# Optimization experiments

Hardware: AMD Instinct MI355X
Metric: run time of the kernel (lower is better)

Reference implementation:

```python
import jax, jax.numpy as jnp
import numpy as np

jax.config.update("jax_enable_x64", True)

C = 62          # in/conv channels
T = 2000        # time samples
B = 256         # batch
VEC_DIM = C * (C + 1) // 2  # 1953
HIDDEN = 64
NUM_CLASSES = 3
SPD_EPS = 1e-3
LOGMAP_EPS = 1e-6


def setup_inputs() -> dict:
    key = jax.random.key(0)
    ks = jax.random.split(key, 8)
    x = jax.random.normal(ks[0], (B, C, T), dtype=jnp.float32)
    # Conv1d kernel_size=1 == per-timestep channel mixing: weight [out_c, in_c]
    conv_w = jax.random.normal(ks[1], (C, C), dtype=jnp.float32) / np.sqrt(C)
    conv_b = jax.random.normal(ks[2], (C,), dtype=jnp.float32) * 0.01
    proj_w = jax.random.normal(ks[3], (HIDDEN, VEC_DIM), dtype=jnp.float32) / np.sqrt(VEC_DIM)
    proj_b = jax.random.normal(ks[4], (HIDDEN,), dtype=jnp.float32) * 0.01
    head_w = jax.random.normal(ks[5], (NUM_CLASSES, HIDDEN), dtype=jnp.float32) / np.sqrt(HIDDEN)
    head_b = jax.random.normal(ks[6], (NUM_CLASSES,), dtype=jnp.float32) * 0.01
    return {"x": x, "conv_w": conv_w, "conv_b": conv_b,
            "proj_w": proj_w, "proj_b": proj_b,
            "head_w": head_w, "head_b": head_b}


def _forward(x, conv_w, conv_b, proj_w, proj_b, head_w, head_b):
    # Conv1d with kernel_size=1: [B,C,T] -> [B,C,T]
    xc = jnp.einsum('oc,bct->bot', conv_w, x) + conv_b[None, :, None]
    # covariance in double precision (torch code does .double())
    xc64 = xc.astype(jnp.float64)
    x_cen = xc64 - xc64.mean(axis=2, keepdims=True)
    denom = float(max(1, T - 1))
    cov = jnp.einsum('bct,bdt->bcd', x_cen, x_cen) / denom  # [B,C,C]
    cov = 0.5 * (cov + jnp.swapaxes(cov, 1, 2))
    # SPD regularization + re-symmetrize
    cov = cov + SPD_EPS * jnp.eye(C, dtype=jnp.float64)
    cov = 0.5 * (cov + jnp.swapaxes(cov, 1, 2))
    # log-map: eigh, clamp, log, reconstruct
    vals, vecs = jnp.linalg.eigh(cov)                       # [B,C], [B,C,C]
    log_vals = jnp.log(jnp.maximum(vals, LOGMAP_EPS))
    log_cov = jnp.einsum('bik,bk,bjk->bij', vecs, log_vals, vecs)
    # upper-triangular (incl. diag) vectorization, row-major like torch.triu_indices
    iu, ju = jnp.triu_indices(C)
    vec = log_cov[:, iu, ju].astype(jnp.float32)            # [B, 1953]
    feat = jax.nn.relu(vec @ proj_w.T + proj_b)             # [B, 64]
    logits = feat @ head_w.T + head_b                       # [B, 3]
    return logits


def reference(x, conv_w, conv_b, proj_w, proj_b, head_w, head_b):
    return _forward(x, conv_w, conv_b, proj_w, proj_b, head_w, head_b)
```

## Files before the change

kernel.cpp:

```cpp
#include <hip/hip_runtime.h>
#include <math.h>

#define CC 62
#define TT 2000
#define BB 256
#define VECN 1953
#define HID 64
#define NCLS 3
#define NG 31
#define LDX 68
#define XBUF (64 * LDX)
#define NT1 32
#define SLD 64
#define LDGF 68

typedef const unsigned int __attribute__((address_space(1)))* gbl_u32p;
typedef unsigned int __attribute__((address_space(3)))* lds_u32p;

#define WAITV(n) asm volatile("s_waitcnt vmcnt(" #n ")" ::: "memory")

__device__ __forceinline__ void decodePi(int pi, int& i, int& j)
{
    int ii = 0, rem = pi;
    while (rem >= CC - ii) { rem -= (CC - ii); ++ii; }
    i = ii; j = ii + rem;
}

__device__ __forceinline__ void pairPQ(int r, int k, int& p, int& q)
{
    if (k == 0) { p = 0; q = 1 + (r + 60) % 61; }
    else {
        p = 1 + (r + k - 1) % 61;
        q = 1 + (r + 60 - k) % 61;
    }
    if (p > q) { int t = p; p = q; q = t; }
}

__global__ __launch_bounds__(576) void fused(
    const float* __restrict__ x, const float* __restrict__ cw,
    const float* __restrict__ pw, const float* __restrict__ pbias,
    const float* __restrict__ hw, const float* __restrict__ hb,
    float* __restrict__ out)
{
    const int b = blockIdx.x, tid = threadIdx.x;
    const int wid = tid >> 6, lane = tid & 63;

    __shared__ __align__(16) double sA[4352];
    __shared__ __align__(16) double sC[VECN];
    __shared__ double sU[9 * 64];
    __shared__ double sNorm[64];
    __shared__ double sD[64];
    __shared__ double sMean[64];
    __shared__ unsigned short sPair[61 * NG];
    __shared__ int    sFlag;
    __shared__ float  sF[HID];

    float*  sX   = reinterpret_cast<float*>(sA);
    double* sS   = sA;
    float*  sGf  = reinterpret_cast<float*>(sA);
    float*  sVec = reinterpret_cast<float*>(sC);

    const int slot = tid >> 2, myks = tid & 3;
    const bool actA = (slot < 136);
    int gi = 0, gj = 0;
    if (actA) {
        int g = 0, rem = slot;
        while (rem >= 16 - g) { rem -= (16 - g); ++g; }
        gi = g; gj = g + rem;
    }
    const int a0 = 4 * gi, b0 = 4 * gj;
    const int pA = gi >> 1, pB = gj >> 1;

    double acc[4][4];
    float  accf[4][4];
#pragma unroll
    for (int r = 0; r < 4; ++r)
#pragma unroll
        for (int c = 0; c < 4; ++c) { acc[r][c] = 0.0; accf[r][c] = 0.0f; }

    for (int e = tid; e < 61 * NG; e += 576) {
        int r = e / NG, k = e - r * NG;
        int p, q; pairPQ(r, k, p, q);
        sPair[e] = (unsigned short)(p | (q << 8));
    }
    if (tid < 128) {
        int bu = tid >> 6, t = tid & 63;
        sX[bu * XBUF + 62 * LDX + t] = 1.0f;
        sX[bu * XBUF + 63 * LDX + t] = 0.0f;
    }
    __syncthreads();

    const float* xb = x + (size_t)b * (CC * TT);

    auto issueTile = [&](int buf, int tile) {
        const int t0 = tile * 64;
        for (int c = wid; c < CC; c += 9) {
            const int ps = c >> 3;
            const int tt = 4 * ((lane >> 2) ^ ps) + (lane & 3);
            if (t0 + tt < TT) {
                const float* gp = xb + (size_t)c * TT + t0 + tt;
                __builtin_amdgcn_global_load_lds(
                    (gbl_u32p)gp, (lds_u32p)&sX[buf * XBUF + c * LDX], 4, 0, 0);
            }
        }
    };

    issueTile(0, 0);
    for (int tile = 0; tile < NT1; ++tile) {
        const int cur = tile & 1;
        __builtin_amdgcn_s_barrier();
        if (tile + 1 < NT1) {
            issueTile(cur ^ 1, tile + 1);
            if (wid < 8) WAITV(7); else WAITV(6);
        } else {
            WAITV(0);
        }
        __builtin_amdgcn_sched_barrier(0);
        __builtin_amdgcn_s_barrier();
        if (actA) {
            const float* xt = &sX[cur * XBUF];
            const int nq = min(16, (TT - tile * 64) >> 2);
            for (int m = myks; m < nq; m += 4) {
                const int ca = 4 * (m ^ pA), cb = 4 * (m ^ pB);
                float4 af[4], bf[4];
#pragma unroll
                for (int r = 0; r < 4; ++r)
                    af[r] = *reinterpret_cast<const float4*>(&xt[(a0 + r) * LDX + ca]);
#pragma unroll
                for (int r = 0; r < 4; ++r)
                    bf[r] = *reinterpret_cast<const float4*>(&xt[(b0 + r) * LDX + cb]);
#pragma unroll
                for (int k = 0; k < 4; ++k) {
#pragma unroll
                    for (int r = 0; r < 4; ++r)
#pragma unroll
                        for (int s = 0; s < 4; ++s)
                            accf[r][s] += (&af[r].x)[k] * (&bf[s].x)[k];
                }
            }
#pragma unroll
            for (int r = 0; r < 4; ++r)
#pragma unroll
                for (int c = 0; c < 4; ++c) {
                    acc[r][c] += (double)accf[r][c];
                    accf[r][c] = 0.0f;
                }
        }
    }

#pragma unroll
    for (int r = 0; r < 4; ++r)
#pragma unroll
        for (int c = 0; c < 4; ++c) {
            double v = acc[r][c];
            v += __shfl_xor(v, 1, 4);
            v += __shfl_xor(v, 2, 4);
            acc[r][c] = v;
        }
    __syncthreads();
    if (actA && myks == 0) {
#pragma unroll
        for (int r = 0; r < 4; ++r)
#pragma unroll
            for (int c = 0; c < 4; ++c)
                sS[(a0 + r) * SLD + (b0 + c)] = acc[r][c];
    }
    __syncthreads();

    if (tid < CC) sMean[tid] = sS[tid * SLD + 62] / (double)TT;
    __syncthreads();

    for (int pi = tid; pi < VECN; pi += 576) {
        int i, j; decodePi(pi, i, j);
        sC[pi] = (sS[i * SLD + j] - (double)TT * sMean[i] * sMean[j]) / 1999.0;
    }
    __syncthreads();

    for (int e = tid; e < CC * LDGF; e += 576) sGf[e] = 0.0f;
    __syncthreads();

    const int jj = tid >> 6, kk = tid & 63;
    for (int j0 = 0; j0 < CC; j0 += 9) {
        const int j = j0 + jj;
        if (kk < CC && j < CC) {
            const float* wr = cw + j * CC;
            double a = 0.0; int idx = kk;
            for (int l = 0; l < kk; ++l) { a += sC[idx] * (double)wr[l]; idx += 61 - l; }
            for (int l = kk; l < CC; ++l) { a += sC[idx] * (double)wr[l]; idx += 1; }
            sU[jj * 64 + kk] = a;
        }
        __syncthreads();
        const int i = kk;
        if (i < CC && j < CC && i <= j) {
            const float* wi = cw + i * CC;
            double a = (i == j) ? 1e-3 : 0.0;
            for (int l = 0; l < CC; ++l) a += (double)wi[l] * sU[jj * 64 + l];
            sGf[j * LDGF + i] = (float)a;
            sGf[i * LDGF + j] = (float)a;
        }
        __syncthreads();
    }

    if (tid < CC) {
        const float* col = &sGf[tid * LDGF];
        double n = 0.0;
        for (int i2 = 0; i2 < CC; ++i2) n += (double)col[i2] * (double)col[i2];
        sNorm[tid] = n;
    }
    __syncthreads();

    const int g = tid >> 4, lt = tid & 15;
    const bool actJ = (g < NG);
    const int r0 = 4 * lt;

    for (int sweep = 0; sweep < 20; ++sweep) {
        if (tid == 0) sFlag = 0;
        __syncthreads();
        for (int r = 0; r < 61; ++r) {
            if (actJ) {
                int pq = sPair[r * NG + g];
                int p = pq & 255, q = pq >> 8;
                float4* gp = reinterpret_cast<float4*>(&sGf[p * LDGF + r0]);
                float4* gq = reinterpret_cast<float4*>(&sGf[q * LDGF + r0]);
                float4 P = *gp, Q = *gq;
                float df = P.x * Q.x + P.y * Q.y + P.z * Q.z + P.w * Q.w;
                { int t2 = __builtin_amdgcn_mov_dpp(__float_as_int(df), 0xB1, 0xF, 0xF, true);
                  df += __int_as_float(t2); }
                { int t2 = __builtin_amdgcn_mov_dpp(__float_as_int(df), 0x4E, 0xF, 0xF, true);
                  df += __int_as_float(t2); }
                { int t2 = __builtin_amdgcn_mov_dpp(__float_as_int(df), 0x141, 0xF, 0xF, true);
                  df += __int_as_float(t2); }
                { int t2 = __builtin_amdgcn_mov_dpp(__float_as_int(df), 0x140, 0xF, 0xF, true);
                  df += __int_as_float(t2); }
                double d = (double)df;
                double np = sNorm[p], nq = sNorm[q];
                if (d * d > np * nq * 1e-12) {
                    float thf = (float)(nq - np) / (2.0f * df);
                    float af2 = fabsf(thf);
                    float tf = 1.0f / (af2 + sqrtf(af2 * af2 + 1.0f));
                    if (thf < 0.0f) tf = -tf;
                    float cf = rsqrtf(tf * tf + 1.0f);
                    float sn = tf * cf;
                    *gp = make_float4(cf * P.x - sn * Q.x, cf * P.y - sn * Q.y,
                                      cf * P.z - sn * Q.z, cf * P.w - sn * Q.w);
                    *gq = make_float4(sn * P.x + cf * Q.x, sn * P.y + cf * Q.y,
                                      sn * P.z + cf * Q.z, sn * P.w + cf * Q.w);
                    if (lt == 0) {
                        double td = (double)tf * d;
                        sNorm[p] = np - td; sNorm[q] = nq + td;
                        sFlag = 1;
                    }
                }
            }
            __syncthreads();
        }
        int flag = sFlag;
        __syncthreads();
        if (!flag) break;
    }

    if (tid < CC) {
        const float* col = &sGf[tid * LDGF];
        double n = 0.0;
        for (int i5 = 0; i5 < CC; ++i5) n += (double)col[i5] * (double)col[i5];
        double lamv = sqrt(n);
        sD[tid] = log(fmax(lamv, 1e-6)) / n;
    }
    __syncthreads();

    for (int pi = tid; pi < VECN; pi += 576) {
        int i, j; decodePi(pi, i, j);
        double a = 0.0;
        for (int k2 = 0; k2 < CC; ++k2)
            a += sD[k2] * (double)sGf[k2 * LDGF + i] * (double)sGf[k2 * LDGF + j];
        sVec[pi] = (float)a;
    }
    __syncthreads();

    if (wid < 8) {
        for (int hh = 0; hh < 8; ++hh) {
            const int h = wid * 8 + hh;
            const float* w = pw + (size_t)h * VECN;
            float a = 0.0f;
            for (int k = lane; k < VECN; k += 64) a += sVec[k] * w[k];
            a += __shfl_xor(a, 32); a += __shfl_xor(a, 16); a += __shfl_xor(a, 8);
            a += __shfl_xor(a, 4);  a += __shfl_xor(a, 2);  a += __shfl_xor(a, 1);
            if (lane == 0) sF[h] = fmaxf(a + pbias[h], 0.0f);
        }
    }
    __syncthreads();
    if (tid < NCLS) {
        float o = hb[tid];
        for (int hh = 0; hh < HID; ++hh) o += sF[hh] * hw[tid * HID + hh];
        out[b * NCLS + tid] = o;
    }
}

extern "C" void kernel_launch(void* const* d_in, const int* in_sizes, int n_in,
                              void* d_out, int out_size, void* d_ws, size_t ws_size,
                              hipStream_t stream)
{
    const float* x  = (const float*)d_in[0];
    const float* cw = (const float*)d_in[1];
    const float* pw = (const float*)d_in[3];
    const float* pb = (const float*)d_in[4];
    const float* hw = (const float*)d_in[5];
    const float* hb = (const float*)d_in[6];
    float* out = (float*)d_out;

    fused<<<BB, 576, 0, stream>>>(x, cw, pw, pb, hw, hb, out);
}
```

Baseline: 690.3 us.

## Use 8x8 register tiles with 16-way time split for covariance GEMM

Restructures the Gram-matrix accumulation so each group of 16 threads owns an 8x8 output tile over all 36 upper-triangle tile pairs, with every thread handling one float4 time slice. The XOR time swizzle is replaced by a per-8-row padded LDS layout, and float-to-double promotion now runs every 4 tiles instead of every tile. The Jacobi rotation uses raw hardware rcp/sqrt/rsq intrinsics, and the sweep convergence flag is set only when rotations exceed a looser threshold. This cuts LDS traffic and conversion overhead per FMA. The trade-offs are higher register pressure from 128 accumulators, more float32 rounding before promotion, and possibly less accurate eigen results from the early stop.

After: 1.063 ms. 53.9% more time.

```diff
diff --git a/kernel.cpp b/kernel.cpp
--- a/kernel.cpp
+++ b/kernel.cpp
@@ -8,11 +8,12 @@
 #define HID 64
 #define NCLS 3
 #define NG 31
-#define LDX 68
-#define XBUF (64 * LDX)
 #define NT1 32
 #define SLD 64
 #define LDGF 68
+#define XBUF 4416
+
+#define RB(c) ((c)*68 + (((c) >> 3) << 3))
 
 typedef const unsigned int __attribute__((address_space(1)))* gbl_u32p;
 typedef unsigned int __attribute__((address_space(3)))* lds_u32p;
@@ -45,7 +46,7 @@
     const int b = blockIdx.x, tid = threadIdx.x;
     const int wid = tid >> 6, lane = tid & 63;
 
-    __shared__ __align__(16) double sA[4352];
+    __shared__ __align__(16) double sA[4416];
     __shared__ __align__(16) double sC[VECN];
     __shared__ double sU[9 * 64];
     __shared__ double sNorm[64];
@@ -60,23 +61,22 @@
     float*  sGf  = reinterpret_cast<float*>(sA);
     float*  sVec = reinterpret_cast<float*>(sC);
 
-    const int slot = tid >> 2, myks = tid & 3;
-    const bool actA = (slot < 136);
+    const int pr = tid >> 4, myks = tid & 15;
     int gi = 0, gj = 0;
-    if (actA) {
-        int g = 0, rem = slot;
-        while (rem >= 16 - g) { rem -= (16 - g); ++g; }
+    {
+        int g = 0, rem = pr;
+        while (rem >= 8 - g) { rem -= (8 - g); ++g; }
         gi = g; gj = g + rem;
     }
-    const int a0 = 4 * gi, b0 = 4 * gj;
-    const int pA = gi >> 1, pB = gj >> 1;
-
-    double acc[4][4];
-    float  accf[4][4];
-#pragma unroll
-    for (int r = 0; r < 4; ++r)
-#pragma unroll
-        for (int c = 0; c < 4; ++c) { acc[r][c] = 0.0; accf[r][c] = 0.0f; }
+    const int a0 = 8 * gi, b0 = 8 * gj;
+    const int baseA = RB(a0), baseB = RB(b0);
+
+    double acc[8][8];
+    float  accf[8][8];
+#pragma unroll
+    for (int r = 0; r < 8; ++r)
+#pragma unroll
+        for (int s = 0; s < 8; ++s) { acc[r][s] = 0.0; accf[r][s] = 0.0f; }
 
     for (int e = tid; e < 61 * NG; e += 576) {
         int r = e / NG, k = e - r * NG;
@@ -85,8 +85,8 @@
     }
     if (tid < 128) {
         int bu = tid >> 6, t = tid & 63;
-        sX[bu * XBUF + 62 * LDX + t] = 1.0f;
-        sX[bu * XBUF + 63 * LDX + t] = 0.0f;
+        sX[bu * XBUF + RB(62) + t] = 1.0f;
+        sX[bu * XBUF + RB(63) + t] = 0.0f;
     }
     __syncthreads();
 
@@ -95,12 +95,10 @@
     auto issueTile = [&](int buf, int tile) {
         const int t0 = tile * 64;
         for (int c = wid; c < CC; c += 9) {
-            const int ps = c >> 3;
-            const int tt = 4 * ((lane >> 2) ^ ps) + (lane & 3);
-            if (t0 + tt < TT) {
-                const float* gp = xb + (size_t)c * TT + t0 + tt;
+            if (t0 + lane < TT) {
+                const float* gp = xb + (size_t)c * TT + t0 + lane;
                 __builtin_amdgcn_global_load_lds(
-                    (gbl_u32p)gp, (lds_u32p)&sX[buf * XBUF + c * LDX], 4, 0, 0);
+                    (gbl_u32p)gp, (lds_u32p)&sX[buf * XBUF + RB(c)], 4, 0, 0);
             }
         }
     };
@@ -117,53 +115,60 @@
         }
         __builtin_amdgcn_sched_barrier(0);
         __builtin_amdgcn_s_barrier();
-        if (actA) {
+        {
             const float* xt = &sX[cur * XBUF];
-            const int nq = min(16, (TT - tile * 64) >> 2);
-            for (int m = myks; m < nq; m += 4) {
-                const int ca = 4 * (m ^ pA), cb = 4 * (m ^ pB);
-                float4 af[4], bf[4];
-#pragma unroll
-                for (int r = 0; r < 4; ++r)
-                    af[r] = *reinterpret_cast<const float4*>(&xt[(a0 + r) * LDX + ca]);
-#pragma unroll
-                for (int r = 0; r < 4; ++r)
-                    bf[r] = *reinterpret_cast<const float4*>(&xt[(b0 + r) * LDX + cb]);
-#pragma unroll
-                for (int k = 0; k < 4; ++k) {
-#pragma unroll
-                    for (int r = 0; r < 4; ++r)
-#pragma unroll
-                        for (int s = 0; s < 4; ++s)
+            const int lim = TT - tile * 64;
+            if (4 * myks < lim) {
+                float4 af[8], bf[8];
+#pragma unroll
+                for (int r = 0; r < 8; ++r)
+                    af[r] = *reinterpret_cast<const float4*>(
+                        &xt[baseA + 68 * r + 4 * myks]);
+#pragma unroll
+                for (int r = 0; r < 8; ++r)
+                    bf[r] = *reinterpret_cast<const float4*>(
+                        &xt[baseB + 68 * r + 4 * myks]);
+#pragma unroll
+                for (int k = 0; k < 4; ++k)
+#pragma unroll
+                    for (int r = 0; r < 8; ++r)
+#pragma unroll
+                        for (int s = 0; s < 8; ++s)
                             accf[r][s] += (&af[r].x)[k] * (&bf[s].x)[k];
-                }
-            }
-#pragma unroll
-            for (int r = 0; r < 4; ++r)
-#pragma unroll
-                for (int c = 0; c < 4; ++c) {
-                    acc[r][c] += (double)accf[r][c];
-                    accf[r][c] = 0.0f;
-                }
-        }
-    }
-
-#pragma unroll
-    for (int r = 0; r < 4; ++r)
-#pragma unroll
-        for (int c = 0; c < 4; ++c) {
-            double v = acc[r][c];
-            v += __shfl_xor(v, 1, 4);
-            v += __shfl_xor(v, 2, 4);
-            acc[r][c] = v;
-        }
-    __syncthreads();
-    if (actA && myks == 0) {
-#pragma unroll
-        for (int r = 0; r < 4; ++r)
-#pragma unroll
-            for (int c = 0; c < 4; ++c)
-                sS[(a0 + r) * SLD + (b0 + c)] = acc[r][c];
+            }
+            if ((tile & 3) == 3) {
+#pragma unroll
+                for (int r = 0; r < 8; ++r)
+#pragma unroll
+                    for (int s = 0; s < 8; ++s) {
+                        acc[r][s] += (double)accf[r][s];
+                        accf[r][s] = 0.0f;
+                    }
+            }
+        }
+    }
+
+#pragma unroll
+    for (int r = 0; r < 8; ++r)
+#pragma unroll
+        for (int s = 0; s < 8; ++s) {
+            double v = acc[r][s];
+            v += __shfl_xor(v, 1, 16);
+            v += __shfl_xor(v, 2, 16);
+            v += __shfl_xor(v, 4, 16);
+            v += __shfl_xor(v, 8, 16);
+            acc[r][s] = v;
+        }
+    __syncthreads();
+    if (myks == 0) {
+#pragma unroll
+        for (int r = 0; r < 8; ++r)
+#pragma unroll
+            for (int s = 0; s < 8; ++s) {
+                int i = a0 + r, j = b0 + s;
+                if (i <= j && j <= 62)
+                    sS[i * SLD + j] = acc[r][s];
+            }
     }
     __syncthreads();
 
@@ -234,12 +239,16 @@
                   df += __int_as_float(t2); }
                 double d = (double)df;
                 double np = sNorm[p], nq = sNorm[q];
-                if (d * d > np * nq * 1e-12) {
-                    float thf = (float)(nq - np) / (2.0f * df);
-                    float af2 = fabsf(thf);
-                    float tf = 1.0f / (af2 + sqrtf(af2 * af2 + 1.0f));
+                double d2 = d * d, bb = np * nq;
+                if (d2 > bb * 1e-12) {
+                    float npf = (float)np, nqf = (float)nq;
+                    float thf = (nqf - npf) *
+                                __builtin_amdgcn_rcpf(2.0f * df);
+                    float a2 = fabsf(thf);
+                    float tf = __builtin_amdgcn_rcpf(
+                        a2 + __builtin_amdgcn_sqrtf(fmaf(a2, a2, 1.0f)));
                     if (thf < 0.0f) tf = -tf;
-                    float cf = rsqrtf(tf * tf + 1.0f);
+                    float cf = __builtin_amdgcn_rsqf(fmaf(tf, tf, 1.0f));
                     float sn = tf * cf;
                     *gp = make_float4(cf * P.x - sn * Q.x, cf * P.y - sn * Q.y,
                                       cf * P.z - sn * Q.z, cf * P.w - sn * Q.w);
@@ -248,7 +257,7 @@
                     if (lt == 0) {
                         double td = (double)tf * d;
                         sNorm[p] = np - td; sNorm[q] = nq + td;
-                        sFlag = 1;
+                        if (d2 > bb * 1e-9) sFlag = 1;
                     }
                 }
             }
```
